# Kernel tuning notes

Measured on AMD Instinct MI355X. Metric: run time of the kernel, lower is better.

The kernel has to match this reference:

```python
import jax, jax.numpy as jnp
import numpy as np

B, N, C = 64, 197, 768
H, GH, D = 12, 2, 64           # num_heads, global_heads, head_dim
HR = H // GH                    # head_ratio = 6
TOTAL_HEADS = 2 * GH + H        # 16
SCALE = D ** -0.5
LEVELS = 3


def setup_inputs() -> dict:
    key = jax.random.key(0)
    ks = jax.random.split(key, 10)
    s = 0.02
    return {
        "x": jax.random.normal(ks[0], (B, N, C), jnp.float32),
        "qkv_w": jax.random.normal(ks[1], (C, TOTAL_HEADS * D), jnp.float32) * s,
        "qkv_b": jax.random.normal(ks[2], (TOTAL_HEADS * D,), jnp.float32) * s,
        "masks": jax.random.uniform(ks[3], (N, N, LEVELS), jnp.float32),
        "mask_proj": jnp.ones((LEVELS, H), jnp.float32),
        "mask_base": jax.random.normal(ks[4], (H,), jnp.float32) * s,
        "head_proj_w": jnp.eye(H, dtype=jnp.float32) + jax.random.normal(ks[5], (H, H), jnp.float32) * s,
        "head_proj_b": jax.random.normal(ks[6], (H,), jnp.float32) * s,
        "proj_w": jax.random.normal(ks[7], (C, C), jnp.float32) * s,
        "proj_b": jax.random.normal(ks[8], (C,), jnp.float32) * s,
    }


def reference(x, qkv_w, qkv_b, masks, mask_proj, mask_base, head_proj_w, head_proj_b, proj_w, proj_b):
    b, n, c = x.shape
    # fused qkv projection -> (b, total_heads, n, d)
    qkv = (x @ qkv_w + qkv_b).reshape(b, n, TOTAL_HEADS, D).transpose(0, 2, 1, 3)
    q = qkv[:, :GH]                 # (b, gh, n, d)
    k = qkv[:, GH:2 * GH]           # (b, gh, n, d)
    v = qkv[:, 2 * GH:]             # (b, h, n, d)

    # global-head attention scores (b, gh, n, n)
    attn = jnp.einsum("bgnd,bgmd->bgnm", q, k) * SCALE

    # per-pair learned mask weights: (n, n, levels) @ (levels, h) -> (n, n, h)
    mw = masks @ mask_proj + mask_base
    # reshape to (1, gh, n, n, hr) per global_proj_type='full'
    mw = mw.reshape(n, n, GH, HR).transpose(2, 0, 1, 3)[None]

    # modulate scores: (b, gh, n, n, hr)
    a = attn[..., None] * mw

    # non_linear head mixing: relu then per-position linear over heads
    a = a.transpose(0, 2, 3, 1, 4).reshape(b, n, n, H)   # (b, n, n, h)
    a = jax.nn.relu(a) @ head_proj_w + head_proj_b
    a = a.transpose(0, 3, 1, 2)                          # (b, h, n, n)

    a = jax.nn.softmax(a, axis=-1)
    out = jnp.einsum("bhnm,bhmd->bnhd", a, v).reshape(b, n, c)
    return out @ proj_w + proj_b
```

## Files before the change

kernel.cpp:

```cpp
#include <hip/hip_runtime.h>
#include <cstdint>
#include <cstddef>

#define BB   64
#define NN   197
#define CC   768
#define HH   12
#define THD  16
#define DD   64
#define MROWS (BB*NN)
#define QKVN (THD*DD)
#define SCALE_ 0.125f
#define ATTS 208
#define KPAD 224
#define SSTR 240

typedef unsigned short u16;
typedef __attribute__((ext_vector_type(2))) float f32x2;
typedef __attribute__((ext_vector_type(4))) float f32x4;
typedef __attribute__((ext_vector_type(8))) short s16x8;
typedef __attribute__((address_space(1))) unsigned int as1_u32;
typedef __attribute__((address_space(3))) unsigned int as3_u32;

__device__ __forceinline__ float bf2f(u16 u) {
  union { unsigned int i; float f; } x; x.i = ((unsigned int)u) << 16; return x.f;
}
__device__ __forceinline__ u16 f2bf(float f) {
  unsigned int x = __builtin_bit_cast(unsigned int, f);
  unsigned int r = (x + 0x7fffu + ((x >> 16) & 1u)) >> 16;
  return (u16)r;
}
__device__ __forceinline__ void gl_lds16(const u16* g, u16* l) {
  __builtin_amdgcn_global_load_lds((const as1_u32*)g, (as3_u32*)l, 16, 0, 0);
}

__global__ __launch_bounds__(256) void k_cvt_x(const float* __restrict__ src,
                                               u16* __restrict__ dst, int n8) {
  int i = blockIdx.x * 256 + threadIdx.x;
  if (i >= n8) return;
  const float4* s = (const float4*)src;
  float4 a = s[2 * i], b = s[2 * i + 1];
  ushort4 lo, hi;
  lo.x = f2bf(a.x); lo.y = f2bf(a.y); lo.z = f2bf(a.z); lo.w = f2bf(a.w);
  hi.x = f2bf(b.x); hi.y = f2bf(b.y); hi.z = f2bf(b.z); hi.w = f2bf(b.w);
  ((ushort4*)dst)[2 * i] = lo;
  ((ushort4*)dst)[2 * i + 1] = hi;
}

__global__ __launch_bounds__(256) void k_transpose(const float* __restrict__ in,
                                                   u16* __restrict__ out,
                                                   int R, int Ccol) {
  __shared__ u16 tile[32][33];
  int c0 = blockIdx.x * 32, r0 = blockIdx.y * 32;
  int tx = threadIdx.x & 31, ty = threadIdx.x >> 5;
#pragma unroll
  for (int i = 0; i < 32; i += 8) {
    int r = r0 + ty + i, c = c0 + tx;
    tile[ty + i][tx] = (r < R && c < Ccol) ? f2bf(in[(size_t)r * Ccol + c]) : (u16)0;
  }
  __syncthreads();
#pragma unroll
  for (int i = 0; i < 32; i += 8) {
    int cc = c0 + ty + i, rr = r0 + tx;
    if (cc < Ccol && rr < R) out[(size_t)cc * R + rr] = tile[tx][ty + i];
  }
}

__global__ __launch_bounds__(512, 2) void k_gemm_bt(const u16* __restrict__ A,
                                                    const u16* __restrict__ Bt,
                                                    const float* __restrict__ bias,
                                                    void* __restrict__ Cout,
                                                    int M, int Nn, int K,
                                                    int write_bf16) {
  __shared__ u16 As[3][256 * 32];
  __shared__ u16 Bs[3][256 * 32];
  int t = threadIdx.x;
  int w = t >> 6, lane = t & 63;

  int NT = gridDim.y;
  int nwg = gridDim.x * gridDim.y;
  int d = blockIdx.y * gridDim.x + blockIdx.x;
  int q8 = nwg >> 3, r8 = nwg & 7;
  int xcd = d & 7, j = d >> 3;
  int g = (xcd < r8 ? xcd * (q8 + 1) : r8 * (q8 + 1) + (xcd - r8) * q8) + j;
  int mt = g / NT, nt_ = g - mt * NT;
  int m0 = mt * 256, n0 = nt_ * 256;

  int wm = w >> 2, wn = w & 3;

  f32x4 acc[8][4];
#pragma unroll
  for (int i = 0; i < 8; i++)
#pragma unroll
    for (int j2 = 0; j2 < 4; j2++)
#pragma unroll
      for (int e = 0; e < 4; e++) acc[i][j2][e] = 0.f;

  int lrow4 = lane >> 2;
  int lkc = (lane & 3) * 8;

  auto stage = [&](int buf, int kk) {
#pragma unroll
    for (int rc = 0; rc < 2; rc++) {
      int c = w + rc * 8;
      int row = c * 16 + lrow4;
      int ga = m0 + row; if (ga >= M) ga = M - 1;
      gl_lds16(A + (size_t)ga * K + kk + lkc, &As[buf][c * 512]);
      gl_lds16(Bt + (size_t)(n0 + row) * K + kk + lkc, &Bs[buf][c * 512]);
    }
  };

  auto compute = [&](int buf) {
    int r16 = lane & 15, k8 = (lane >> 4) * 8;
    s16x8 af[8], bfv[4];
#pragma unroll
    for (int s = 0; s < 8; s++)
      af[s] = *(const s16x8*)&As[buf][(wm * 128 + s * 16 + r16) * 32 + k8];
#pragma unroll
    for (int s = 0; s < 4; s++)
      bfv[s] = *(const s16x8*)&Bs[buf][(wn * 64 + s * 16 + r16) * 32 + k8];
#pragma unroll
    for (int sm = 0; sm < 8; sm++)
#pragma unroll
      for (int sn = 0; sn < 4; sn++)
        acc[sm][sn] = __builtin_amdgcn_mfma_f32_16x16x32_bf16(af[sm], bfv[sn], acc[sm][sn], 0, 0, 0);
  };

  int nt = K >> 5;
  stage(0, 0);
  stage(1, 32);
  for (int tt = 0; tt < nt - 2; ++tt) {
    stage((tt + 2) % 3, (tt + 2) * 32);
    asm volatile("s_waitcnt vmcnt(8)" ::: "memory");
    __builtin_amdgcn_sched_barrier(0);
    __builtin_amdgcn_s_barrier();
    compute(tt % 3);
    __builtin_amdgcn_s_barrier();
  }
  asm volatile("s_waitcnt vmcnt(4)" ::: "memory");
  __builtin_amdgcn_sched_barrier(0);
  __builtin_amdgcn_s_barrier();
  compute((nt - 2) % 3);
  __builtin_amdgcn_s_barrier();
  asm volatile("s_waitcnt vmcnt(0)" ::: "memory");
  __builtin_amdgcn_sched_barrier(0);
  __builtin_amdgcn_s_barrier();
  compute((nt - 1) % 3);

  u16*   Cb = (u16*)Cout;
  float* Cf = (float*)Cout;
  int quad = lane >> 4, col = lane & 15;
#pragma unroll
  for (int sn = 0; sn < 4; sn++) {
    int gn = n0 + wn * 64 + sn * 16 + col;
    float bv = bias[gn];
#pragma unroll
    for (int sm = 0; sm < 8; sm++) {
      int gmb = m0 + wm * 128 + sm * 16 + quad * 4;
#pragma unroll
      for (int i = 0; i < 4; i++) {
        int gm = gmb + i;
        if (gm < M) {
          float v = acc[sm][sn][i] + bv;
          if (write_bf16) Cb[(size_t)gm * Nn + gn] = f2bf(v);
          else            Cf[(size_t)gm * Nn + gn] = v;
        }
      }
    }
  }
}

__global__ __launch_bounds__(256) void k_qk(const u16* __restrict__ qkv,
                                            float* __restrict__ att) {
  __shared__ u16 As[2][128 * 32];
  __shared__ u16 Bs[2][128 * 32];
  int t = threadIdx.x;
  int w = t >> 6, lane = t & 63;
  int bz = blockIdx.z, b = bz >> 1, g = bz & 1;
  int n0 = blockIdx.x * 128;
  int m0 = blockIdx.y * 128;
  int wm = w >> 1, wn = w & 1;

  f32x4 acc[4][4];
#pragma unroll
  for (int i = 0; i < 4; i++)
#pragma unroll
    for (int j = 0; j < 4; j++)
#pragma unroll
      for (int e = 0; e < 4; e++) acc[i][j][e] = 0.f;

  int lrow4 = lane >> 2, lkc = (lane & 3) * 8;

#pragma unroll
  for (int half = 0; half < 2; half++) {
    int kk = half * 32;
#pragma unroll
    for (int rc = 0; rc < 2; rc++) {
      int c = w + rc * 4;
      int row = c * 16 + lrow4;
      int nq = n0 + row; if (nq > NN - 1) nq = NN - 1;
      int mk = m0 + row; if (mk > NN - 1) mk = NN - 1;
      gl_lds16(qkv + (size_t)(b * NN + nq) * QKVN + g * DD + kk + lkc, &As[half][c * 512]);
      gl_lds16(qkv + (size_t)(b * NN + mk) * QKVN + 2 * DD + g * DD + kk + lkc, &Bs[half][c * 512]);
    }
  }
  __syncthreads();
  {
    int r16 = lane & 15, k8 = (lane >> 4) * 8;
#pragma unroll
    for (int half = 0; half < 2; half++) {
      s16x8 af[4], bfv[4];
#pragma unroll
      for (int s = 0; s < 4; s++) {
        af[s]  = *(const s16x8*)&As[half][(wm * 64 + s * 16 + r16) * 32 + k8];
        bfv[s] = *(const s16x8*)&Bs[half][(wn * 64 + s * 16 + r16) * 32 + k8];
      }
#pragma unroll
      for (int sm = 0; sm < 4; sm++)
#pragma unroll
        for (int sn = 0; sn < 4; sn++)
          acc[sm][sn] = __builtin_amdgcn_mfma_f32_16x16x32_bf16(af[sm], bfv[sn], acc[sm][sn], 0, 0, 0);
    }
  }
  int quad = lane >> 4, col = lane & 15;
#pragma unroll
  for (int sn = 0; sn < 4; sn++) {
    int gn = m0 + wn * 64 + sn * 16 + col;
#pragma unroll
    for (int sm = 0; sm < 4; sm++) {
      int gmb = n0 + wm * 64 + sm * 16 + quad * 4;
#pragma unroll
      for (int i = 0; i < 4; i++) {
        int gm = gmb + i;
        if (gm < NN && gn < NN)
          att[((size_t)bz * NN + gm) * ATTS + gn] = acc[sm][sn][i] * SCALE_;
      }
    }
  }
}

__global__ __launch_bounds__(256) void k_softmax_p(const float* __restrict__ att,
                                                   const float* __restrict__ masks,
                                                   const float* __restrict__ mproj,
                                                   const float* __restrict__ mbase,
                                                   const float* __restrict__ hpw,
                                                   const float* __restrict__ hpb,
                                                   u16* __restrict__ P) {
  __shared__ float S[12][SSTR];
  __shared__ f32x2 hpw_s[72];
  __shared__ f32x2 mp_s[18];
  __shared__ f32x2 mb_s[6], hpb_s[6];
  __shared__ float inv_s[12];
  int t = threadIdx.x;
  int n = blockIdx.x, b = blockIdx.y;

  if (t < 72) hpw_s[t] = ((const f32x2*)hpw)[t];
  if (t < 18) mp_s[t] = ((const f32x2*)mproj)[t];
  if (t < 6) { mb_s[t] = ((const f32x2*)mbase)[t]; hpb_s[t] = ((const f32x2*)hpb)[t]; }
  __syncthreads();

  if (t < NN) {
    int m = t;
    float a0 = att[((size_t)(b * 2 + 0) * NN + n) * ATTS + m];
    float a1 = att[((size_t)(b * 2 + 1) * NN + n) * ATTS + m];
    const float* mk = masks + ((size_t)n * NN + m) * 3;
    float l0 = mk[0], l1 = mk[1], l2 = mk[2];
    f32x2 pre2[6];
#pragma unroll
    for (int k = 0; k < 6; k++) {
      f32x2 wv = mb_s[k] + l0 * mp_s[k] + l1 * mp_s[6 + k] + l2 * mp_s[12 + k];
      float av = (k < 3) ? a0 : a1;
      f32x2 v = wv * av;
      pre2[k].x = v.x > 0.f ? v.x : 0.f;
      pre2[k].y = v.y > 0.f ? v.y : 0.f;
    }
    f32x2 s2[6];
#pragma unroll
    for (int k = 0; k < 6; k++) s2[k] = hpb_s[k];
#pragma unroll
    for (int h = 0; h < 12; h++) {
      float p = (h & 1) ? pre2[h >> 1].y : pre2[h >> 1].x;
#pragma unroll
      for (int k = 0; k < 6; k++) s2[k] += p * hpw_s[h * 6 + k];
    }
#pragma unroll
    for (int k = 0; k < 6; k++) {
      S[2 * k][m] = s2[k].x;
      S[2 * k + 1][m] = s2[k].y;
    }
  } else if (t < KPAD) {
#pragma unroll
    for (int h = 0; h < 12; h++) S[h][t] = 0.f;
  }
  __syncthreads();

  {
    int g = t >> 4, l16 = t & 15;
    if (g < 12) {
      float vals[13];
      float mx = -1e30f;
#pragma unroll
      for (int i = 0; i < 13; i++) {
        int m = l16 + i * 16;
        float x = S[g][m];
        vals[i] = (m < NN) ? x : -1e30f;
        mx = fmaxf(mx, vals[i]);
      }
#pragma unroll
      for (int off = 8; off; off >>= 1) mx = fmaxf(mx, __shfl_xor(mx, off, 16));
      float sum = 0.f;
#pragma unroll
      for (int i = 0; i < 13; i++) {
        int m = l16 + i * 16;
        float e = __expf(vals[i] - mx);
        if (m < NN) { S[g][m] = e; sum += e; }
      }
#pragma unroll
      for (int off = 8; off; off >>= 1) sum += __shfl_xor(sum, off, 16);
      if (l16 == 0) inv_s[g] = 1.f / sum;
    }
  }
  __syncthreads();

  for (int c4 = t; c4 < 672; c4 += 256) {
    int h = c4 / 56;
    int m = (c4 - h * 56) * 4;
    f32x4 v = *(const f32x4*)&S[h][m];
    float iv = inv_s[h];
    ushort4 u;
    u.x = f2bf(v.x * iv); u.y = f2bf(v.y * iv);
    u.z = f2bf(v.z * iv); u.w = f2bf(v.w * iv);
    *(ushort4*)(P + ((size_t)(b * HH + h) * NN + n) * KPAD + m) = u;
  }
}

__global__ __launch_bounds__(256) void k_pv(const u16* __restrict__ P,
                                            const u16* __restrict__ qkv,
                                            u16* __restrict__ aout) {
  __shared__ u16 As[2][128 * 32];
  __shared__ u16 Bs[2][64 * 32];
  int t = threadIdx.x;
  int w = t >> 6, lane = t & 63;
  int bh = blockIdx.y, b = bh / HH, h = bh - b * HH;
  int n0 = blockIdx.x * 128;

  f32x4 acc[2][4];
#pragma unroll
  for (int i = 0; i < 2; i++)
#pragma unroll
    for (int j = 0; j < 4; j++)
#pragma unroll
      for (int e = 0; e < 4; e++) acc[i][j][e] = 0.f;

  int lrow4 = lane >> 2, lkc = (lane & 3) * 8;
  int vml = t & 31, vd0 = (t >> 5) * 8;

  for (int k0 = 0; k0 < KPAD; k0 += 64) {
    int nh = (KPAD - k0 >= 64) ? 2 : 1;
    for (int half = 0; half < nh; half++) {
      int kk = k0 + half * 32;
#pragma unroll
      for (int rc = 0; rc < 2; rc++) {
        int c = w + rc * 4;
        int row = c * 16 + lrow4;
        int gn = n0 + row; if (gn > NN - 1) gn = NN - 1;
        gl_lds16(P + ((size_t)bh * NN + gn) * KPAD + kk + lkc, &As[half][c * 512]);
      }
      {
        int m = kk + vml;
        u16 v8[8];
        if (m < NN) {
          const ushort4* vp = (const ushort4*)(qkv + (size_t)(b * NN + m) * QKVN + (4 + h) * DD + vd0);
          ushort4 lo = vp[0], hi = vp[1];
          v8[0] = lo.x; v8[1] = lo.y; v8[2] = lo.z; v8[3] = lo.w;
          v8[4] = hi.x; v8[5] = hi.y; v8[6] = hi.z; v8[7] = hi.w;
        } else {
#pragma unroll
          for (int j = 0; j < 8; j++) v8[j] = 0;
        }
#pragma unroll
        for (int j = 0; j < 8; j++) Bs[half][(vd0 + j) * 32 + vml] = v8[j];
      }
    }
    __syncthreads();
    int r16 = lane & 15, k8 = (lane >> 4) * 8;
    for (int half = 0; half < nh; half++) {
      s16x8 af[2], bfv[4];
#pragma unroll
      for (int s = 0; s < 2; s++)
        af[s] = *(const s16x8*)&As[half][(w * 32 + s * 16 + r16) * 32 + k8];
#pragma unroll
      for (int s = 0; s < 4; s++)
        bfv[s] = *(const s16x8*)&Bs[half][(s * 16 + r16) * 32 + k8];
#pragma unroll
      for (int sm = 0; sm < 2; sm++)
#pragma unroll
        for (int sn = 0; sn < 4; sn++)
          acc[sm][sn] = __builtin_amdgcn_mfma_f32_16x16x32_bf16(af[sm], bfv[sn], acc[sm][sn], 0, 0, 0);
    }
    __syncthreads();
  }
  int quad = lane >> 4, col = lane & 15;
#pragma unroll
  for (int sn = 0; sn < 4; sn++) {
    int gd = sn * 16 + col;
#pragma unroll
    for (int sm = 0; sm < 2; sm++) {
      int gnb = n0 + w * 32 + sm * 16 + quad * 4;
#pragma unroll
      for (int i = 0; i < 4; i++) {
        int gn = gnb + i;
        if (gn < NN)
          aout[(size_t)(b * NN + gn) * CC + h * DD + gd] = f2bf(acc[sm][sn][i]);
      }
    }
  }
}

extern "C" void kernel_launch(void* const* d_in, const int* in_sizes, int n_in,
                              void* d_out, int out_size, void* d_ws, size_t ws_size,
                              hipStream_t stream) {
  const float* x     = (const float*)d_in[0];
  const float* qkv_w = (const float*)d_in[1];
  const float* qkv_b = (const float*)d_in[2];
  const float* masks = (const float*)d_in[3];
  const float* mproj = (const float*)d_in[4];
  const float* mbase = (const float*)d_in[5];
  const float* hpw   = (const float*)d_in[6];
  const float* hpb   = (const float*)d_in[7];
  const float* projw = (const float*)d_in[8];
  const float* projb = (const float*)d_in[9];

  char* ws = (char*)d_ws;
  size_t off = 0;
  auto alloc = [&](size_t bytes) {
    char* p = ws + off; off = (off + bytes + 255) & ~(size_t)255; return p;
  };
  char*  r1   = alloc((size_t)BB * 2 * NN * ATTS * 4);
  u16*   xbf  = (u16*)r1;
  float* att  = (float*)r1;
  u16*   aout = (u16*)r1;
  u16*   qkv  = (u16*)alloc((size_t)MROWS * QKVN * 2);
  u16*   P    = (u16*)alloc((size_t)BB * HH * NN * KPAD * 2);
  u16*   wt1  = (u16*)alloc((size_t)QKVN * CC * 2);
  u16*   wt2  = (u16*)alloc((size_t)CC * CC * 2);

  int n8 = MROWS * CC / 8;
  k_cvt_x<<<(n8 + 255) / 256, 256, 0, stream>>>(x, xbf, n8);
  k_transpose<<<dim3(QKVN / 32, CC / 32), 256, 0, stream>>>(qkv_w, wt1, CC, QKVN);
  k_transpose<<<dim3(CC / 32, CC / 32), 256, 0, stream>>>(projw, wt2, CC, CC);
  k_gemm_bt<<<dim3((MROWS + 255) / 256, QKVN / 256), 512, 0, stream>>>(
      xbf, wt1, qkv_b, qkv, MROWS, QKVN, CC, 1);
  k_qk<<<dim3(2, 2, BB * 2), 256, 0, stream>>>(qkv, att);
  k_softmax_p<<<dim3(NN, BB), 256, 0, stream>>>(att, masks, mproj, mbase, hpw, hpb, P);
  k_pv<<<dim3(2, BB * HH), 256, 0, stream>>>(P, qkv, aout);
  k_gemm_bt<<<dim3((MROWS + 255) / 256, CC / 256), 512, 0, stream>>>(
      aout, wt2, projb, d_out, MROWS, CC, CC, 0);
}
```

Baseline: 274.3 us.

## Fuse QK, mask-mix softmax and PV into one attention kernel

Replaces the separate QK-score, softmax/P-materialization and PV kernels with a single fused attention kernel per (batch, 32-row query tile). It computes scores in LDS, applies the mask weights and head mixing, exponentiates without a max subtraction, and feeds bf16 P straight into the PV MFMAs, normalizing at the end. The QKV GEMM epilogue now writes V transposed into a padded buffer, and the mask-weight projection is precomputed by a small kernel. This removes the global round-trips of fp32 scores and the bf16 P matrix. The costs are skipping max-subtraction (overflow risk for large logits), scattered transposed V stores, an extra memset, and the GEMM launch bound dropping to one block per CU.

```diff
diff --git a/kernel.cpp b/kernel.cpp
--- a/kernel.cpp
+++ b/kernel.cpp
@@ -12,13 +12,13 @@
 #define QKVN (THD*DD)
 #define SCALE_ 0.125f
 #define ATTS 208
-#define KPAD 224
-#define SSTR 240
+#define VTSTR 256
 
 typedef unsigned short u16;
 typedef __attribute__((ext_vector_type(2))) float f32x2;
 typedef __attribute__((ext_vector_type(4))) float f32x4;
 typedef __attribute__((ext_vector_type(8))) short s16x8;
+typedef __attribute__((ext_vector_type(2))) unsigned int u32x2;
 typedef __attribute__((address_space(1))) unsigned int as1_u32;
 typedef __attribute__((address_space(3))) unsigned int as3_u32;
 
@@ -66,10 +66,23 @@
   }
 }
 
-__global__ __launch_bounds__(512, 2) void k_gemm_bt(const u16* __restrict__ A,
+__global__ __launch_bounds__(256) void k_mw(const float* __restrict__ masks,
+                                            const float* __restrict__ mproj,
+                                            const float* __restrict__ mbase,
+                                            float* __restrict__ mw12) {
+  int i = blockIdx.x * 256 + threadIdx.x;
+  if (i >= NN * NN) return;
+  float l0 = masks[(size_t)i * 3], l1 = masks[(size_t)i * 3 + 1], l2 = masks[(size_t)i * 3 + 2];
+#pragma unroll
+  for (int h = 0; h < 12; h++)
+    mw12[(size_t)i * 12 + h] = mbase[h] + l0 * mproj[h] + l1 * mproj[12 + h] + l2 * mproj[24 + h];
+}
+
+__global__ __launch_bounds__(512, 1) void k_gemm_bt(const u16* __restrict__ A,
                                                     const u16* __restrict__ Bt,
                                                     const float* __restrict__ bias,
                                                     void* __restrict__ Cout,
+                                                    u16* __restrict__ vt,
                                                     int M, int Nn, int K,
                                                     int write_bf16) {
   __shared__ u16 As[3][256 * 32];
@@ -162,256 +175,229 @@
         int gm = gmb + i;
         if (gm < M) {
           float v = acc[sm][sn][i] + bv;
-          if (write_bf16) Cb[(size_t)gm * Nn + gn] = f2bf(v);
-          else            Cf[(size_t)gm * Nn + gn] = v;
-        }
-      }
-    }
-  }
-}
-
-__global__ __launch_bounds__(256) void k_qk(const u16* __restrict__ qkv,
-                                            float* __restrict__ att) {
-  __shared__ u16 As[2][128 * 32];
-  __shared__ u16 Bs[2][128 * 32];
+          if (write_bf16) {
+            if (vt && gn >= 2 * 2 * DD) {
+              int bidx = gm / NN, mrow = gm - bidx * NN;
+              int hh = (gn - 256) >> 6, dd = gn & 63;
+              vt[(((size_t)bidx * HH + hh) * DD + dd) * VTSTR + mrow] = f2bf(v);
+            } else {
+              Cb[(size_t)gm * Nn + gn] = f2bf(v);
+            }
+          } else {
+            Cf[(size_t)gm * Nn + gn] = v;
+          }
+        }
+      }
+    }
+  }
+}
+
+__global__ __launch_bounds__(512, 1) void k_attn(const u16* __restrict__ qkv,
+                                                 const u16* __restrict__ vt,
+                                                 const float* __restrict__ mw12,
+                                                 const float* __restrict__ hpw,
+                                                 const float* __restrict__ hpb,
+                                                 u16* __restrict__ aout) {
+  __shared__ u16 Qs[8 * 512];
+  __shared__ u16 Ks[2][16 * 512];
+  __shared__ u16 Ps[48 * 512];
+  __shared__ u16 VTs[32 * 512];
+  __shared__ float S[2 * 32 * 68];
+  __shared__ float inv_s[12 * 32];
+  __shared__ f32x2 hpw_s[72];
+  __shared__ f32x2 hpb_s[6];
+
   int t = threadIdx.x;
   int w = t >> 6, lane = t & 63;
-  int bz = blockIdx.z, b = bz >> 1, g = bz & 1;
-  int n0 = blockIdx.x * 128;
-  int m0 = blockIdx.y * 128;
-  int wm = w >> 1, wn = w & 1;
-
-  f32x4 acc[4][4];
-#pragma unroll
-  for (int i = 0; i < 4; i++)
-#pragma unroll
-    for (int j = 0; j < 4; j++)
-#pragma unroll
-      for (int e = 0; e < 4; e++) acc[i][j][e] = 0.f;
-
-  int lrow4 = lane >> 2, lkc = (lane & 3) * 8;
-
-#pragma unroll
-  for (int half = 0; half < 2; half++) {
-    int kk = half * 32;
+  int bI = blockIdx.x & 63;
+  int n0 = (blockIdx.x >> 6) * 32;
+
+  if (t < 72) hpw_s[t] = ((const f32x2*)hpw)[t];
+  if (t < 6)  hpb_s[t] = ((const f32x2*)hpb)[t];
+
+  int r16 = lane & 15, k8 = (lane >> 4) * 8;
+  int quad = lane >> 4, col = lane & 15;
+
+  auto stageK = [&](int buf, int mm0) {
 #pragma unroll
     for (int rc = 0; rc < 2; rc++) {
-      int c = w + rc * 4;
-      int row = c * 16 + lrow4;
-      int nq = n0 + row; if (nq > NN - 1) nq = NN - 1;
-      int mk = m0 + row; if (mk > NN - 1) mk = NN - 1;
-      gl_lds16(qkv + (size_t)(b * NN + nq) * QKVN + g * DD + kk + lkc, &As[half][c * 512]);
-      gl_lds16(qkv + (size_t)(b * NN + mk) * QKVN + 2 * DD + g * DD + kk + lkc, &Bs[half][c * 512]);
-    }
-  }
+      int c = w + rc * 8;
+      int gg = c >> 3, kh = (c >> 2) & 1, mc = c & 3;
+      int m = mm0 + mc * 16 + (lane >> 2); if (m > NN - 1) m = NN - 1;
+      int k = kh * 32 + (lane & 3) * 8;
+      gl_lds16(qkv + (size_t)(bI * NN + m) * QKVN + 2 * DD + gg * DD + k,
+               &Ks[buf][c * 512]);
+    }
+  };
+
+  {
+    int gg = w >> 2, kh = (w >> 1) & 1, nc = w & 1;
+    int n = n0 + nc * 16 + (lane >> 2); if (n > NN - 1) n = NN - 1;
+    int k = kh * 32 + (lane & 3) * 8;
+    gl_lds16(qkv + (size_t)(bI * NN + n) * QKVN + gg * DD + k, &Qs[w * 512]);
+  }
+  stageK(0, 0);
   __syncthreads();
-  {
-    int r16 = lane & 15, k8 = (lane >> 4) * 8;
-#pragma unroll
-    for (int half = 0; half < 2; half++) {
-      s16x8 af[4], bfv[4];
-#pragma unroll
-      for (int s = 0; s < 4; s++) {
-        af[s]  = *(const s16x8*)&As[half][(wm * 64 + s * 16 + r16) * 32 + k8];
-        bfv[s] = *(const s16x8*)&Bs[half][(wn * 64 + s * 16 + r16) * 32 + k8];
-      }
-#pragma unroll
-      for (int sm = 0; sm < 4; sm++)
-#pragma unroll
-        for (int sn = 0; sn < 4; sn++)
-          acc[sm][sn] = __builtin_amdgcn_mfma_f32_16x16x32_bf16(af[sm], bfv[sn], acc[sm][sn], 0, 0, 0);
-    }
-  }
-  int quad = lane >> 4, col = lane & 15;
-#pragma unroll
-  for (int sn = 0; sn < 4; sn++) {
-    int gn = m0 + wn * 64 + sn * 16 + col;
-#pragma unroll
-    for (int sm = 0; sm < 4; sm++) {
-      int gmb = n0 + wm * 64 + sm * 16 + quad * 4;
+
+  int pn = t >> 4, tm = t & 15;
+  int nG = n0 + pn; if (nG > NN - 1) nG = NN - 1;
+  int pr = pn & 15, pnc = pn >> 4;
+
+  f32x2 lsum[6];
+#pragma unroll
+  for (int k = 0; k < 6; k++) { lsum[k].x = 0.f; lsum[k].y = 0.f; }
+
+  f32x4 accPV[3][4];
+#pragma unroll
+  for (int u = 0; u < 3; u++)
+#pragma unroll
+    for (int s = 0; s < 4; s++)
+#pragma unroll
+      for (int e = 0; e < 4; e++) accPV[u][s][e] = 0.f;
+
+  int qg = w >> 2, mq = w & 3;
+  int hh8 = w >> 1, nh = w & 1;
+
+  for (int mt = 0; mt < 4; ++mt) {
+    int m0 = mt * 64;
+    int cur = mt & 1;
+
+    {
+      f32x4 qa[2];
+#pragma unroll
+      for (int nc = 0; nc < 2; nc++)
+#pragma unroll
+        for (int e = 0; e < 4; e++) qa[nc][e] = 0.f;
+#pragma unroll
+      for (int kh = 0; kh < 2; kh++) {
+        s16x8 bk = *(const s16x8*)&Ks[cur][((qg * 2 + kh) * 4 + mq) * 512 + r16 * 32 + k8];
+#pragma unroll
+        for (int nc = 0; nc < 2; nc++) {
+          s16x8 aq = *(const s16x8*)&Qs[((qg * 2 + kh) * 2 + nc) * 512 + r16 * 32 + k8];
+          qa[nc] = __builtin_amdgcn_mfma_f32_16x16x32_bf16(aq, bk, qa[nc], 0, 0, 0);
+        }
+      }
+#pragma unroll
+      for (int nc = 0; nc < 2; nc++)
+#pragma unroll
+        for (int i = 0; i < 4; i++)
+          S[(qg * 32 + nc * 16 + quad * 4 + i) * 68 + mq * 16 + col] = qa[nc][i] * SCALE_;
+    }
+    __syncthreads();
+
+    if (mt < 3) stageK(cur ^ 1, m0 + 64);
+
+    {
+      const f32x4* S4 = (const f32x4*)S;
+      f32x4 s0 = S4[pn * 17 + tm];
+      f32x4 s1 = S4[(32 + pn) * 17 + tm];
+      int gm0 = m0 + tm * 4;
+      int gmc = gm0 > NN - 1 ? NN - 1 : gm0;
+      const f32x4* mwp = (const f32x4*)(mw12 + ((size_t)nG * NN + gmc) * 12);
+      unsigned int pk[12][2];
+#pragma unroll
+      for (int h = 0; h < 12; h++) { pk[h][0] = 0u; pk[h][1] = 0u; }
+#pragma unroll
+      for (int j = 0; j < 4; j++) {
+        int valid = (gm0 + j) < NN;
+        f32x4 w0 = mwp[j * 3 + 0], w1 = mwp[j * 3 + 1], w2 = mwp[j * 3 + 2];
+        float a0 = s0[j], a1 = s1[j];
+        f32x2 pre[6];
+        pre[0] = *(const f32x2*)&w0 * a0;
+        pre[1] = *((const f32x2*)&w0 + 1) * a0;
+        pre[2] = *(const f32x2*)&w1 * a0;
+        pre[3] = *((const f32x2*)&w1 + 1) * a1;
+        pre[4] = *(const f32x2*)&w2 * a1;
+        pre[5] = *((const f32x2*)&w2 + 1) * a1;
+#pragma unroll
+        for (int k = 0; k < 6; k++) {
+          pre[k].x = pre[k].x > 0.f ? pre[k].x : 0.f;
+          pre[k].y = pre[k].y > 0.f ? pre[k].y : 0.f;
+        }
+        f32x2 a12[6];
+#pragma unroll
+        for (int k = 0; k < 6; k++) a12[k] = hpb_s[k];
+#pragma unroll
+        for (int h = 0; h < 12; h++) {
+          float p = (h & 1) ? pre[h >> 1].y : pre[h >> 1].x;
+#pragma unroll
+          for (int k = 0; k < 6; k++) a12[k] += p * hpw_s[h * 6 + k];
+        }
+#pragma unroll
+        for (int k = 0; k < 6; k++) {
+          float ex = 0.f, ey = 0.f;
+          if (valid) {
+            ex = __expf(a12[k].x); ey = __expf(a12[k].y);
+            lsum[k].x += ex; lsum[k].y += ey;
+          }
+          pk[2 * k][j >> 1]     |= (unsigned int)f2bf(ex) << ((j & 1) * 16);
+          pk[2 * k + 1][j >> 1] |= (unsigned int)f2bf(ey) << ((j & 1) * 16);
+        }
+      }
+      int mh = tm >> 3;
+#pragma unroll
+      for (int h = 0; h < 12; h++) {
+        u32x2 val; val.x = pk[h][0]; val.y = pk[h][1];
+        *(u32x2*)&Ps[((h * 2 + mh) * 2 + pnc) * 512 + pr * 32 + (tm & 7) * 4] = val;
+      }
+    }
+    __syncthreads();
+
+    for (int bt = 0; bt < 3; ++bt) {
+#pragma unroll
+      for (int cc = 0; cc < 4; ++cc) {
+        int c = w * 4 + cc;
+        int vh = c >> 3, vmh = (c >> 2) & 1, dc = c & 3;
+        int h = bt * 4 + vh;
+        int dd = dc * 16 + (lane >> 2);
+        int m = m0 + vmh * 32 + (lane & 3) * 8;
+        gl_lds16(vt + (((size_t)bI * HH + h) * DD + dd) * VTSTR + m, &VTs[c * 512]);
+      }
+      __syncthreads();
+      {
+        int h = bt * 4 + hh8;
+#pragma unroll
+        for (int mh = 0; mh < 2; mh++) {
+          s16x8 pa = *(const s16x8*)&Ps[((h * 2 + mh) * 2 + nh) * 512 + r16 * 32 + k8];
+#pragma unroll
+          for (int s = 0; s < 4; s++) {
+            s16x8 vb = *(const s16x8*)&VTs[((hh8 * 2 + mh) * 4 + s) * 512 + r16 * 32 + k8];
+            accPV[bt][s] = __builtin_amdgcn_mfma_f32_16x16x32_bf16(pa, vb, accPV[bt][s], 0, 0, 0);
+          }
+        }
+      }
+      __syncthreads();
+    }
+  }
+
+#pragma unroll
+  for (int off = 8; off; off >>= 1)
+#pragma unroll
+    for (int k = 0; k < 6; k++) {
+      lsum[k].x += __shfl_xor(lsum[k].x, off, 16);
+      lsum[k].y += __shfl_xor(lsum[k].y, off, 16);
+    }
+  if (tm == 0) {
+#pragma unroll
+    for (int k = 0; k < 6; k++) {
+      inv_s[(2 * k) * 32 + pn]     = 1.f / lsum[k].x;
+      inv_s[(2 * k + 1) * 32 + pn] = 1.f / lsum[k].y;
+    }
+  }
+  __syncthreads();
+
+#pragma unroll
+  for (int bt = 0; bt < 3; ++bt) {
+    int h = bt * 4 + hh8;
+    f32x4 iv = *(const f32x4*)&inv_s[h * 32 + nh * 16 + quad * 4];
+#pragma unroll
+    for (int s = 0; s < 4; s++) {
 #pragma unroll
       for (int i = 0; i < 4; i++) {
-        int gm = gmb + i;
-        if (gm < NN && gn < NN)
-          att[((size_t)bz * NN + gm) * ATTS + gn] = acc[sm][sn][i] * SCALE_;
-      }
-    }
-  }
-}
-
-__global__ __launch_bounds__(256) void k_softmax_p(const float* __restrict__ att,
-                                                   const float* __restrict__ masks,
-                                                   const float* __restrict__ mproj,
-                                                   const float* __restrict__ mbase,
-                                                   const float* __restrict__ hpw,
-                                                   const float* __restrict__ hpb,
-                                                   u16* __restrict__ P) {
-  __shared__ float S[12][SSTR];
-  __shared__ f32x2 hpw_s[72];
-  __shared__ f32x2 mp_s[18];
-  __shared__ f32x2 mb_s[6], hpb_s[6];
-  __shared__ float inv_s[12];
-  int t = threadIdx.x;
-  int n = blockIdx.x, b = blockIdx.y;
-
-  if (t < 72) hpw_s[t] = ((const f32x2*)hpw)[t];
-  if (t < 18) mp_s[t] = ((const f32x2*)mproj)[t];
-  if (t < 6) { mb_s[t] = ((const f32x2*)mbase)[t]; hpb_s[t] = ((const f32x2*)hpb)[t]; }
-  __syncthreads();
-
-  if (t < NN) {
-    int m = t;
-    float a0 = att[((size_t)(b * 2 + 0) * NN + n) * ATTS + m];
-    float a1 = att[((size_t)(b * 2 + 1) * NN + n) * ATTS + m];
-    const float* mk = masks + ((size_t)n * NN + m) * 3;
-    float l0 = mk[0], l1 = mk[1], l2 = mk[2];
-    f32x2 pre2[6];
-#pragma unroll
-    for (int k = 0; k < 6; k++) {
-      f32x2 wv = mb_s[k] + l0 * mp_s[k] + l1 * mp_s[6 + k] + l2 * mp_s[12 + k];
-      float av = (k < 3) ? a0 : a1;
-      f32x2 v = wv * av;
-      pre2[k].x = v.x > 0.f ? v.x : 0.f;
-      pre2[k].y = v.y > 0.f ? v.y : 0.f;
-    }
-    f32x2 s2[6];
-#pragma unroll
-    for (int k = 0; k < 6; k++) s2[k] = hpb_s[k];
-#pragma unroll
-    for (int h = 0; h < 12; h++) {
-      float p = (h & 1) ? pre2[h >> 1].y : pre2[h >> 1].x;
-#pragma unroll
-      for (int k = 0; k < 6; k++) s2[k] += p * hpw_s[h * 6 + k];
-    }
-#pragma unroll
-    for (int k = 0; k < 6; k++) {
-      S[2 * k][m] = s2[k].x;
-      S[2 * k + 1][m] = s2[k].y;
-    }
-  } else if (t < KPAD) {
-#pragma unroll
-    for (int h = 0; h < 12; h++) S[h][t] = 0.f;
-  }
-  __syncthreads();
-
-  {
-    int g = t >> 4, l16 = t & 15;
-    if (g < 12) {
-      float vals[13];
-      float mx = -1e30f;
-#pragma unroll
-      for (int i = 0; i < 13; i++) {
-        int m = l16 + i * 16;
-        float x = S[g][m];
-        vals[i] = (m < NN) ? x : -1e30f;
-        mx = fmaxf(mx, vals[i]);
-      }
-#pragma unroll
-      for (int off = 8; off; off >>= 1) mx = fmaxf(mx, __shfl_xor(mx, off, 16));
-      float sum = 0.f;
-#pragma unroll
-      for (int i = 0; i < 13; i++) {
-        int m = l16 + i * 16;
-        float e = __expf(vals[i] - mx);
-        if (m < NN) { S[g][m] = e; sum += e; }
-      }
-#pragma unroll
-      for (int off = 8; off; off >>= 1) sum += __shfl_xor(sum, off, 16);
-      if (l16 == 0) inv_s[g] = 1.f / sum;
-    }
-  }
-  __syncthreads();
-
-  for (int c4 = t; c4 < 672; c4 += 256) {
-    int h = c4 / 56;
-    int m = (c4 - h * 56) * 4;
-    f32x4 v = *(const f32x4*)&S[h][m];
-    float iv = inv_s[h];
-    ushort4 u;
-    u.x = f2bf(v.x * iv); u.y = f2bf(v.y * iv);
-    u.z = f2bf(v.z * iv); u.w = f2bf(v.w * iv);
-    *(ushort4*)(P + ((size_t)(b * HH + h) * NN + n) * KPAD + m) = u;
-  }
-}
-
-__global__ __launch_bounds__(256) void k_pv(const u16* __restrict__ P,
-                                            const u16* __restrict__ qkv,
-                                            u16* __restrict__ aout) {
-  __shared__ u16 As[2][128 * 32];
-  __shared__ u16 Bs[2][64 * 32];
-  int t = threadIdx.x;
-  int w = t >> 6, lane = t & 63;
-  int bh = blockIdx.y, b = bh / HH, h = bh - b * HH;
-  int n0 = blockIdx.x * 128;
-
-  f32x4 acc[2][4];
-#pragma unroll
-  for (int i = 0; i < 2; i++)
-#pragma unroll
-    for (int j = 0; j < 4; j++)
-#pragma unroll
-      for (int e = 0; e < 4; e++) acc[i][j][e] = 0.f;
-
-  int lrow4 = lane >> 2, lkc = (lane & 3) * 8;
-  int vml = t & 31, vd0 = (t >> 5) * 8;
-
-  for (int k0 = 0; k0 < KPAD; k0 += 64) {
-    int nh = (KPAD - k0 >= 64) ? 2 : 1;
-    for (int half = 0; half < nh; half++) {
-      int kk = k0 + half * 32;
-#pragma unroll
-      for (int rc = 0; rc < 2; rc++) {
-        int c = w + rc * 4;
-        int row = c * 16 + lrow4;
-        int gn = n0 + row; if (gn > NN - 1) gn = NN - 1;
-        gl_lds16(P + ((size_t)bh * NN + gn) * KPAD + kk + lkc, &As[half][c * 512]);
-      }
-      {
-        int m = kk + vml;
-        u16 v8[8];
-        if (m < NN) {
-          const ushort4* vp = (const ushort4*)(qkv + (size_t)(b * NN + m) * QKVN + (4 + h) * DD + vd0);
-          ushort4 lo = vp[0], hi = vp[1];
-          v8[0] = lo.x; v8[1] = lo.y; v8[2] = lo.z; v8[3] = lo.w;
-          v8[4] = hi.x; v8[5] = hi.y; v8[6] = hi.z; v8[7] = hi.w;
-        } else {
-#pragma unroll
-          for (int j = 0; j < 8; j++) v8[j] = 0;
-        }
-#pragma unroll
-        for (int j = 0; j < 8; j++) Bs[half][(vd0 + j) * 32 + vml] = v8[j];
-      }
-    }
-    __syncthreads();
-    int r16 = lane & 15, k8 = (lane >> 4) * 8;
-    for (int half = 0; half < nh; half++) {
-      s16x8 af[2], bfv[4];
-#pragma unroll
-      for (int s = 0; s < 2; s++)
-        af[s] = *(const s16x8*)&As[half][(w * 32 + s * 16 + r16) * 32 + k8];
-#pragma unroll
-      for (int s = 0; s < 4; s++)
-        bfv[s] = *(const s16x8*)&Bs[half][(s * 16 + r16) * 32 + k8];
-#pragma unroll
-      for (int sm = 0; sm < 2; sm++)
-#pragma unroll
-        for (int sn = 0; sn < 4; sn++)
-          acc[sm][sn] = __builtin_amdgcn_mfma_f32_16x16x32_bf16(af[sm], bfv[sn], acc[sm][sn], 0, 0, 0);
-    }
-    __syncthreads();
-  }
-  int quad = lane >> 4, col = lane & 15;
-#pragma unroll
-  for (int sn = 0; sn < 4; sn++) {
-    int gd = sn * 16 + col;
-#pragma unroll
-    for (int sm = 0; sm < 2; sm++) {
-      int gnb = n0 + w * 32 + sm * 16 + quad * 4;
-#pragma unroll
-      for (int i = 0; i < 4; i++) {
-        int gn = gnb + i;
-        if (gn < NN)
-          aout[(size_t)(b * NN + gn) * CC + h * DD + gd] = f2bf(acc[sm][sn][i]);
+        int gnn = n0 + nh * 16 + quad * 4 + i;
+        if (gnn < NN)
+          aout[(size_t)(bI * NN + gnn) * CC + h * DD + s * 16 + col] =
+              f2bf(accPV[bt][s][i] * iv[i]);
       }
     }
   }
@@ -438,22 +424,24 @@
   };
   char*  r1   = alloc((size_t)BB * 2 * NN * ATTS * 4);
   u16*   xbf  = (u16*)r1;
-  float* att  = (float*)r1;
   u16*   aout = (u16*)r1;
   u16*   qkv  = (u16*)alloc((size_t)MROWS * QKVN * 2);
-  u16*   P    = (u16*)alloc((size_t)BB * HH * NN * KPAD * 2);
   u16*   wt1  = (u16*)alloc((size_t)QKVN * CC * 2);
   u16*   wt2  = (u16*)alloc((size_t)CC * CC * 2);
+  size_t vtbytes = (size_t)BB * HH * DD * VTSTR * 2;
+  u16*   vt   = (u16*)alloc(vtbytes);
+  float* mw12 = (float*)alloc((size_t)NN * NN * 12 * 4 + 1024);
+
+  hipMemsetAsync(vt, 0, vtbytes, stream);
 
   int n8 = MROWS * CC / 8;
   k_cvt_x<<<(n8 + 255) / 256, 256, 0, stream>>>(x, xbf, n8);
   k_transpose<<<dim3(QKVN / 32, CC / 32), 256, 0, stream>>>(qkv_w, wt1, CC, QKVN);
   k_transpose<<<dim3(CC / 32, CC / 32), 256, 0, stream>>>(projw, wt2, CC, CC);
+  k_mw<<<(NN * NN + 255) / 256, 256, 0, stream>>>(masks, mproj, mbase, mw12);
   k_gemm_bt<<<dim3((MROWS + 255) / 256, QKVN / 256), 512, 0, stream>>>(
-      xbf, wt1, qkv_b, qkv, MROWS, QKVN, CC, 1);
-  k_qk<<<dim3(2, 2, BB * 2), 256, 0, stream>>>(qkv, att);
-  k_softmax_p<<<dim3(NN, BB), 256, 0, stream>>>(att, masks, mproj, mbase, hpw, hpb, P);
-  k_pv<<<dim3(2, BB * HH), 256, 0, stream>>>(P, qkv, aout);
+      xbf, wt1, qkv_b, qkv, vt, MROWS, QKVN, CC, 1);
+  k_attn<<<dim3(7 * BB), 512, 0, stream>>>(qkv, vt, mw12, hpw, hpb, aout);
   k_gemm_bt<<<dim3((MROWS + 255) / 256, CC / 256), 512, 0, stream>>>(
-      aout, wt2, projb, d_out, MROWS, CC, CC, 0);
-}
+      aout, wt2, projb, d_out, nullptr, MROWS, CC, CC, 0);
+}
```

Result: slower. 342.3 us (+24.8%).

## Stage GEMM and PV epilogues through LDS for vectorized bf16 stores; merge PV row tiles

Applied to the files above, without the earlier changes.

The bf16 output path of the QKV GEMM now writes accumulators into shared memory and then emits 16-byte coalesced row stores, replacing scattered 2-byte stores. The PV kernel now has one block per (batch, head) covering all 197 query rows, which halves the number of V tile loads and transposes. Its output also goes through LDS for vectorized writes. The costs are extra barriers and LDS traffic, fewer PV blocks (768), and more accumulator registers per thread.

```diff
diff --git a/kernel.cpp b/kernel.cpp
--- a/kernel.cpp
+++ b/kernel.cpp
@@ -72,8 +72,9 @@
                                                     void* __restrict__ Cout,
                                                     int M, int Nn, int K,
                                                     int write_bf16) {
-  __shared__ u16 As[3][256 * 32];
-  __shared__ u16 Bs[3][256 * 32];
+  __shared__ u16 SHG[49152];
+  u16* As = SHG;
+  u16* Bs = SHG + 24576;
   int t = threadIdx.x;
   int w = t >> 6, lane = t & 63;
 
@@ -105,8 +106,8 @@
       int c = w + rc * 8;
       int row = c * 16 + lrow4;
       int ga = m0 + row; if (ga >= M) ga = M - 1;
-      gl_lds16(A + (size_t)ga * K + kk + lkc, &As[buf][c * 512]);
-      gl_lds16(Bt + (size_t)(n0 + row) * K + kk + lkc, &Bs[buf][c * 512]);
+      gl_lds16(A + (size_t)ga * K + kk + lkc, &As[buf * 8192 + c * 512]);
+      gl_lds16(Bt + (size_t)(n0 + row) * K + kk + lkc, &Bs[buf * 8192 + c * 512]);
     }
   };
 
@@ -115,10 +116,10 @@
     s16x8 af[8], bfv[4];
 #pragma unroll
     for (int s = 0; s < 8; s++)
-      af[s] = *(const s16x8*)&As[buf][(wm * 128 + s * 16 + r16) * 32 + k8];
+      af[s] = *(const s16x8*)&As[buf * 8192 + (wm * 128 + s * 16 + r16) * 32 + k8];
 #pragma unroll
     for (int s = 0; s < 4; s++)
-      bfv[s] = *(const s16x8*)&Bs[buf][(wn * 64 + s * 16 + r16) * 32 + k8];
+      bfv[s] = *(const s16x8*)&Bs[buf * 8192 + (wn * 64 + s * 16 + r16) * 32 + k8];
 #pragma unroll
     for (int sm = 0; sm < 8; sm++)
 #pragma unroll
@@ -147,23 +148,52 @@
   __builtin_amdgcn_s_barrier();
   compute((nt - 1) % 3);
 
-  u16*   Cb = (u16*)Cout;
-  float* Cf = (float*)Cout;
   int quad = lane >> 4, col = lane & 15;
-#pragma unroll
-  for (int sn = 0; sn < 4; sn++) {
-    int gn = n0 + wn * 64 + sn * 16 + col;
-    float bv = bias[gn];
-#pragma unroll
-    for (int sm = 0; sm < 8; sm++) {
-      int gmb = m0 + wm * 128 + sm * 16 + quad * 4;
-#pragma unroll
-      for (int i = 0; i < 4; i++) {
-        int gm = gmb + i;
+  if (write_bf16) {
+    u16* Cb = (u16*)Cout;
+    u16* O = SHG;
+    __syncthreads();
+#pragma unroll
+    for (int p = 0; p < 2; p++) {
+      if (wm == p) {
+#pragma unroll
+        for (int sn = 0; sn < 4; sn++) {
+          int gn = n0 + wn * 64 + sn * 16 + col;
+          float bv = bias[gn];
+#pragma unroll
+          for (int sm = 0; sm < 8; sm++)
+#pragma unroll
+            for (int i = 0; i < 4; i++)
+              O[(sm * 16 + quad * 4 + i) * 272 + wn * 64 + sn * 16 + col] =
+                  f2bf(acc[sm][sn][i] + bv);
+        }
+      }
+      __syncthreads();
+#pragma unroll
+      for (int it = 0; it < 8; it++) {
+        int q = t + it * 512;
+        int rl = q >> 5, c8 = q & 31;
+        int gm = m0 + p * 128 + rl;
         if (gm < M) {
-          float v = acc[sm][sn][i] + bv;
-          if (write_bf16) Cb[(size_t)gm * Nn + gn] = f2bf(v);
-          else            Cf[(size_t)gm * Nn + gn] = v;
+          s16x8 v = *(const s16x8*)&O[rl * 272 + c8 * 8];
+          *(s16x8*)&Cb[(size_t)gm * Nn + n0 + c8 * 8] = v;
+        }
+      }
+      __syncthreads();
+    }
+  } else {
+    float* Cf = (float*)Cout;
+#pragma unroll
+    for (int sn = 0; sn < 4; sn++) {
+      int gn = n0 + wn * 64 + sn * 16 + col;
+      float bv = bias[gn];
+#pragma unroll
+      for (int sm = 0; sm < 8; sm++) {
+        int gmb = m0 + wm * 128 + sm * 16 + quad * 4;
+#pragma unroll
+        for (int i = 0; i < 4; i++) {
+          int gm = gmb + i;
+          if (gm < M) Cf[(size_t)gm * Nn + gn] = acc[sm][sn][i] + bv;
         }
       }
     }
@@ -337,16 +367,16 @@
 __global__ __launch_bounds__(256) void k_pv(const u16* __restrict__ P,
                                             const u16* __restrict__ qkv,
                                             u16* __restrict__ aout) {
-  __shared__ u16 As[2][128 * 32];
-  __shared__ u16 Bs[2][64 * 32];
+  __shared__ u16 SH[18432];
+  u16* As = SH;
+  u16* Bs = SH + 14336;
   int t = threadIdx.x;
   int w = t >> 6, lane = t & 63;
-  int bh = blockIdx.y, b = bh / HH, h = bh - b * HH;
-  int n0 = blockIdx.x * 128;
-
-  f32x4 acc[2][4];
-#pragma unroll
-  for (int i = 0; i < 2; i++)
+  int bh = blockIdx.x, b = bh / HH, h = bh - b * HH;
+
+  f32x4 acc[4][4];
+#pragma unroll
+  for (int i = 0; i < 4; i++)
 #pragma unroll
     for (int j = 0; j < 4; j++)
 #pragma unroll
@@ -360,11 +390,13 @@
     for (int half = 0; half < nh; half++) {
       int kk = k0 + half * 32;
 #pragma unroll
-      for (int rc = 0; rc < 2; rc++) {
+      for (int rc = 0; rc < 4; rc++) {
         int c = w + rc * 4;
-        int row = c * 16 + lrow4;
-        int gn = n0 + row; if (gn > NN - 1) gn = NN - 1;
-        gl_lds16(P + ((size_t)bh * NN + gn) * KPAD + kk + lkc, &As[half][c * 512]);
+        if (c < 14) {
+          int row = c * 16 + lrow4;
+          int gn = row > NN - 1 ? NN - 1 : row;
+          gl_lds16(P + ((size_t)bh * NN + gn) * KPAD + kk + lkc, &As[half * 7168 + c * 512]);
+        }
       }
       {
         int m = kk + vml;
@@ -379,41 +411,48 @@
           for (int j = 0; j < 8; j++) v8[j] = 0;
         }
 #pragma unroll
-        for (int j = 0; j < 8; j++) Bs[half][(vd0 + j) * 32 + vml] = v8[j];
+        for (int j = 0; j < 8; j++) Bs[half * 2048 + (vd0 + j) * 32 + vml] = v8[j];
       }
     }
     __syncthreads();
     int r16 = lane & 15, k8 = (lane >> 4) * 8;
     for (int half = 0; half < nh; half++) {
-      s16x8 af[2], bfv[4];
-#pragma unroll
-      for (int s = 0; s < 2; s++)
-        af[s] = *(const s16x8*)&As[half][(w * 32 + s * 16 + r16) * 32 + k8];
+      s16x8 bfv[4];
 #pragma unroll
       for (int s = 0; s < 4; s++)
-        bfv[s] = *(const s16x8*)&Bs[half][(s * 16 + r16) * 32 + k8];
-#pragma unroll
-      for (int sm = 0; sm < 2; sm++)
-#pragma unroll
-        for (int sn = 0; sn < 4; sn++)
-          acc[sm][sn] = __builtin_amdgcn_mfma_f32_16x16x32_bf16(af[sm], bfv[sn], acc[sm][sn], 0, 0, 0);
+        bfv[s] = *(const s16x8*)&Bs[half * 2048 + (s * 16 + r16) * 32 + k8];
+#pragma unroll
+      for (int si = 0; si < 4; si++) {
+        int smt = w + si * 4;
+        if (smt < 14) {
+          s16x8 af = *(const s16x8*)&As[half * 7168 + (smt * 16 + r16) * 32 + k8];
+#pragma unroll
+          for (int sn = 0; sn < 4; sn++)
+            acc[si][sn] = __builtin_amdgcn_mfma_f32_16x16x32_bf16(af, bfv[sn], acc[si][sn], 0, 0, 0);
+        }
+      }
     }
     __syncthreads();
   }
+
   int quad = lane >> 4, col = lane & 15;
-#pragma unroll
-  for (int sn = 0; sn < 4; sn++) {
-    int gd = sn * 16 + col;
-#pragma unroll
-    for (int sm = 0; sm < 2; sm++) {
-      int gnb = n0 + w * 32 + sm * 16 + quad * 4;
-#pragma unroll
-      for (int i = 0; i < 4; i++) {
-        int gn = gnb + i;
-        if (gn < NN)
-          aout[(size_t)(b * NN + gn) * CC + h * DD + gd] = f2bf(acc[sm][sn][i]);
-      }
-    }
+  u16* O = SH;
+#pragma unroll
+  for (int si = 0; si < 4; si++) {
+    int smt = w + si * 4;
+    if (smt < 14) {
+#pragma unroll
+      for (int sn = 0; sn < 4; sn++)
+#pragma unroll
+        for (int i = 0; i < 4; i++)
+          O[(smt * 16 + quad * 4 + i) * 80 + sn * 16 + col] = f2bf(acc[si][sn][i]);
+    }
+  }
+  __syncthreads();
+  for (int q = t; q < NN * 8; q += 256) {
+    int rl = q >> 3, c8 = q & 7;
+    s16x8 v = *(const s16x8*)&O[rl * 80 + c8 * 8];
+    *(s16x8*)&aout[(size_t)(b * NN + rl) * CC + h * DD + c8 * 8] = v;
   }
 }
 
@@ -453,7 +492,7 @@
       xbf, wt1, qkv_b, qkv, MROWS, QKVN, CC, 1);
   k_qk<<<dim3(2, 2, BB * 2), 256, 0, stream>>>(qkv, att);
   k_softmax_p<<<dim3(NN, BB), 256, 0, stream>>>(att, masks, mproj, mbase, hpw, hpb, P);
-  k_pv<<<dim3(2, BB * HH), 256, 0, stream>>>(P, qkv, aout);
+  k_pv<<<dim3(BB * HH), 256, 0, stream>>>(P, qkv, aout);
   k_gemm_bt<<<dim3((MROWS + 255) / 256, CC / 256), 512, 0, stream>>>(
       aout, wt2, projb, d_out, MROWS, CC, CC, 0);
 }
```

New measurement: 244.2 us. 11.0% less time.
